# Performance work log

Hardware: AMD Instinct MI355X
Metric: run time of the kernel (lower is better)

Reference implementation:

```python
import jax, jax.numpy as jnp
import numpy as np

HEADS = 12
EPS = 1e-5

def setup_inputs() -> dict:
    key = jax.random.key(0)
    ks = jax.random.split(key, 24)
    B, T, H = 128, 128, 768
    RIN, RH, NT = 512, 512, 10
    s = 0.02
    inp = {
        'slot_vector': jax.random.normal(ks[0], (B, H), jnp.float32),
        'utt_vectors': jax.random.normal(ks[1], (B, T, H), jnp.float32),
        'Wq': jax.random.normal(ks[2], (H, H), jnp.float32) * s,
        'bq': jnp.zeros((H,), jnp.float32),
        'Wk': jax.random.normal(ks[3], (H, H), jnp.float32) * s,
        'bk': jnp.zeros((H,), jnp.float32),
        'Wv': jax.random.normal(ks[4], (H, H), jnp.float32) * s,
        'bv': jnp.zeros((H,), jnp.float32),
        'Wo': jax.random.normal(ks[5], (H, H), jnp.float32) * s,
        'bo': jnp.zeros((H,), jnp.float32),
        'W_in': jax.random.normal(ks[6], (RIN, 2 * H), jnp.float32) * s,
        'b_in': jnp.zeros((RIN,), jnp.float32),
        'W_ih': jax.random.normal(ks[7], (4 * RH, RIN), jnp.float32) * s,
        'W_hh': jax.random.normal(ks[8], (4 * RH, RH), jnp.float32) * s,
        'b_ih': jnp.zeros((4 * RH,), jnp.float32),
        'b_hh': jnp.zeros((4 * RH,), jnp.float32),
        'W_tag': jax.random.normal(ks[9], (NT, RH), jnp.float32) * s,
        'b_tag': jnp.zeros((NT,), jnp.float32),
        'ln_g': jnp.ones((NT,), jnp.float32),
        'ln_b': jnp.zeros((NT,), jnp.float32),
    }
    return inp

def _forward(slot_vector, utt_vectors, Wq, bq, Wk, bk, Wv, bv, Wo, bo,
             W_in, b_in, W_ih, W_hh, b_ih, b_hh, W_tag, b_tag, ln_g, ln_b):
    B, T, H = utt_vectors.shape
    dk = H // HEADS
    # Multi-head attention: Q is slot vector (seq len 1), K/V are utt encodings
    q = (slot_vector @ Wq.T + bq).reshape(B, 1, HEADS, dk).transpose(0, 2, 1, 3)  # [B,h,1,dk]
    k = (utt_vectors @ Wk.T + bk).reshape(B, T, HEADS, dk).transpose(0, 2, 1, 3)  # [B,h,T,dk]
    v = (utt_vectors @ Wv.T + bv).reshape(B, T, HEADS, dk).transpose(0, 2, 1, 3)
    scores = jnp.einsum('bhqd,bhkd->bhqk', q, k) / jnp.sqrt(jnp.float32(dk))
    attn = jax.nn.softmax(scores, axis=-1)
    X = jnp.einsum('bhqk,bhkd->bhqd', attn, v).transpose(0, 2, 1, 3).reshape(B, H)
    X = X @ Wo.T + bo  # [B, H] context vector, fixed across timesteps
    RH = W_hh.shape[1]
    h0 = jnp.zeros((B, RH), jnp.float32)
    c0 = jnp.zeros((B, RH), jnp.float32)

    def step(carry, x_t):
        h, c = carry
        lstm_in = jax.nn.sigmoid(jnp.concatenate([x_t, X], axis=1) @ W_in.T + b_in)
        gates = lstm_in @ W_ih.T + b_ih + h @ W_hh.T + b_hh  # [B, 4*RH]
        i_g, f_g, g_g, o_g = jnp.split(gates, 4, axis=1)  # torch gate order i,f,g,o
        c = jax.nn.sigmoid(f_g) * c + jax.nn.sigmoid(i_g) * jnp.tanh(g_g)
        h = jax.nn.sigmoid(o_g) * jnp.tanh(c)
        y = h @ W_tag.T + b_tag  # [B, NT]
        mu = jnp.mean(y, axis=-1, keepdims=True)
        var = jnp.mean((y - mu) ** 2, axis=-1, keepdims=True)
        y = (y - mu) / jnp.sqrt(var + EPS) * ln_g + ln_b
        return (h, c), y

    xs = utt_vectors.transpose(1, 0, 2)  # [T, B, H]
    _, ys = jax.lax.scan(step, (h0, c0), xs)  # ys: [T, B, NT]
    return ys.transpose(1, 2, 0)  # [B, NT, T]

def reference(slot_vector, utt_vectors, Wq, bq, Wk, bk, Wv, bv, Wo, bo,
              W_in, b_in, W_ih, W_hh, b_ih, b_hh, W_tag, b_tag, ln_g, ln_b):
    return _forward(slot_vector, utt_vectors, Wq, bq, Wk, bk, Wv, bv, Wo, bo,
                    W_in, b_in, W_ih, W_hh, b_ih, b_hh, W_tag, b_tag, ln_g, ln_b)
```

## Files before the change

kernel.cpp:

```cpp
#include <hip/hip_runtime.h>
#include <hip/hip_bf16.h>
#include <math.h>

#define Bc 128
#define Tc 128
#define Hc 768
#define NHEAD 12
#define DKc 64
#define RHc 512
#define G4c 2048
#define NTc 10
#define LNEPS 1e-5f
#define NSLC 16

typedef short bf16x8 __attribute__((ext_vector_type(8)));
typedef float f32x4 __attribute__((ext_vector_type(4)));

__device__ __forceinline__ float sigmoidf_(float x) { return 1.0f / (1.0f + expf(-x)); }

__device__ __forceinline__ ushort f2bf(float f) {
  union { float f; uint u; } c; c.f = f;
  uint r = (c.u + 0x7FFFu + ((c.u >> 16) & 1u)) >> 16;
  return (ushort)r;
}
__device__ __forceinline__ float bf2f(ushort u) {
  union { uint u; float f; } c; c.u = ((uint)u) << 16;
  return c.f;
}
__device__ __forceinline__ uint pack2(float a, float b) {
  return (uint)f2bf(a) | ((uint)f2bf(b) << 16);
}

__global__ void bias_sum_k(const float* __restrict__ a, const float* __restrict__ b,
                           float* __restrict__ o) {
  int i = blockIdx.x * blockDim.x + threadIdx.x;
  if (i < G4c) o[i] = a[i] + b[i];
}

__global__ void cvt4_k(const float* __restrict__ x, ushort* __restrict__ y, int n4) {
  int i = blockIdx.x * 256 + threadIdx.x;
  if (i < n4) {
    float4 v = ((const float4*)x)[i];
    ushort4 o; o.x = f2bf(v.x); o.y = f2bf(v.y); o.z = f2bf(v.z); o.w = f2bf(v.w);
    ((ushort4*)y)[i] = o;
  }
}

__global__ __launch_bounds__(256) void cvt_whh_frag_k(
    const float* __restrict__ Whh, ushort* __restrict__ out)
{
  const int idx = blockIdx.x * 256 + threadIdx.x;
  const int lane = idx & 63;
  const int kf = (idx >> 6) & 15;
  const int sw = idx >> 10;
  const int m = lane & 15;
  const int u = (sw >> 3) * 32 + (sw & 7) * 4 + (m >> 2);
  const int gate = m & 3;
  const int k0 = kf * 32 + (lane >> 4) * 8;
  const float* src = Whh + ((size_t)(gate * RHc + u)) * RHc + k0;
  ushort4 o0, o1;
  o0.x = f2bf(src[0]); o0.y = f2bf(src[1]); o0.z = f2bf(src[2]); o0.w = f2bf(src[3]);
  o1.x = f2bf(src[4]); o1.y = f2bf(src[5]); o1.z = f2bf(src[6]); o1.w = f2bf(src[7]);
  ushort* dst = out + (size_t)idx * 8;
  *(ushort4*)dst = o0;
  *(ushort4*)(dst + 4) = o1;
}

__global__ __launch_bounds__(256) void bgemm_bt(
    const void* __restrict__ Aptr, const ushort* __restrict__ Wb,
    const float* __restrict__ bias, void* __restrict__ Cptr,
    int M, int N, int K, int amode, int outMode,
    const float* __restrict__ utt, const float* __restrict__ xo, int trow0)
{
  __shared__ ushort As[128 * 40];
  __shared__ ushort Ws[128 * 40];
  const int tid = threadIdx.x;
  const int lane = tid & 63, wid = tid >> 6;
  const int wm = wid >> 1, wn = wid & 1;
  const int row0 = blockIdx.y * 128, col0 = blockIdx.x * 128;

  f32x4 acc[4][4];
#pragma unroll
  for (int i = 0; i < 4; ++i)
#pragma unroll
    for (int j = 0; j < 4; ++j) {
      f32x4 z = {0.f, 0.f, 0.f, 0.f};
      acc[i][j] = z;
    }

  const int r = tid >> 1, kq = (tid & 1) * 16;

  for (int kb = 0; kb < K; kb += 32) {
    const int k = kb + kq;
    if (amode == 2) {
      const ushort* ap = (const ushort*)Aptr + (size_t)(row0 + r) * K + k;
      *(uint4*)&As[r * 40 + kq] = *(const uint4*)ap;
      *(uint4*)&As[r * 40 + kq + 8] = *(const uint4*)(ap + 8);
    } else {
      const float* ap;
      if (amode == 0) {
        ap = (const float*)Aptr + (size_t)(row0 + r) * K + k;
      } else {
        const int b = r;
        const int t = trow0 + blockIdx.y;
        ap = (k < Hc) ? utt + ((size_t)b * Tc + t) * Hc + k
                      : xo + (size_t)b * Hc + (k - Hc);
      }
      const float4 f0 = *(const float4*)ap;
      const float4 f1 = *(const float4*)(ap + 4);
      const float4 f2 = *(const float4*)(ap + 8);
      const float4 f3 = *(const float4*)(ap + 12);
      uint4 u0, u1;
      u0.x = pack2(f0.x, f0.y); u0.y = pack2(f0.z, f0.w);
      u0.z = pack2(f1.x, f1.y); u0.w = pack2(f1.z, f1.w);
      u1.x = pack2(f2.x, f2.y); u1.y = pack2(f2.z, f2.w);
      u1.z = pack2(f3.x, f3.y); u1.w = pack2(f3.z, f3.w);
      *(uint4*)&As[r * 40 + kq] = u0;
      *(uint4*)&As[r * 40 + kq + 8] = u1;
    }
    {
      const ushort* wp = Wb + (size_t)(col0 + r) * K + k;
      *(uint4*)&Ws[r * 40 + kq] = *(const uint4*)wp;
      *(uint4*)&Ws[r * 40 + kq + 8] = *(const uint4*)(wp + 8);
    }
    __syncthreads();
    const int koff = (lane >> 4) * 8;
    const int ar = wm * 64 + (lane & 15);
    const int wr = wn * 64 + (lane & 15);
    bf16x8 af[4], wf[4];
#pragma unroll
    for (int i = 0; i < 4; ++i) af[i] = *(const bf16x8*)&As[(ar + i * 16) * 40 + koff];
#pragma unroll
    for (int i = 0; i < 4; ++i) wf[i] = *(const bf16x8*)&Ws[(wr + i * 16) * 40 + koff];
#pragma unroll
    for (int fm = 0; fm < 4; ++fm)
#pragma unroll
      for (int fn = 0; fn < 4; ++fn)
        acc[fm][fn] = __builtin_amdgcn_mfma_f32_16x16x32_bf16(af[fm], wf[fn], acc[fm][fn], 0, 0, 0);
    __syncthreads();
  }

#pragma unroll
  for (int fm = 0; fm < 4; ++fm) {
    const int m0 = row0 + wm * 64 + fm * 16 + ((lane >> 4) * 4);
#pragma unroll
    for (int fn = 0; fn < 4; ++fn) {
      const int n = col0 + wn * 64 + fn * 16 + (lane & 15);
      const float bb = bias[n];
#pragma unroll
      for (int q = 0; q < 4; ++q) {
        const float v = acc[fm][fn][q] + bb;
        if (outMode == 1)
          ((ushort*)Cptr)[(size_t)(m0 + q) * N + n] = f2bf(sigmoidf_(v));
        else
          ((float*)Cptr)[(size_t)(m0 + q) * N + n] = v;
      }
    }
  }
}

__global__ __launch_bounds__(256) void fold_qp_k(
    const float* __restrict__ slot, const float* __restrict__ Wq,
    const float* __restrict__ bq, const float* __restrict__ Wk,
    const float* __restrict__ bk, ushort* __restrict__ Pb, float* __restrict__ cqB)
{
  __shared__ float ss[Hc];
  __shared__ float qp[4][DKc];
  __shared__ float qs[DKc];
  const int bx = blockIdx.x;
  const int b = bx / NHEAD, h = bx % NHEAD;
  const int tid = threadIdx.x;
  for (int i = tid; i < Hc; i += 256) ss[i] = slot[(size_t)b * Hc + i];
  __syncthreads();
  {
    const int d = tid & 63, qt = tid >> 6;
    const float* wr = Wq + (size_t)(h * DKc + d) * Hc + qt * 192;
    const float* sb = ss + qt * 192;
    float a = 0.f;
    for (int e = 0; e < 192; e += 4) {
      const float4 wv = *(const float4*)(wr + e);
      a += wv.x * sb[e] + wv.y * sb[e + 1] + wv.z * sb[e + 2] + wv.w * sb[e + 3];
    }
    qp[qt][d] = a;
  }
  __syncthreads();
  if (tid < DKc)
    qs[tid] = qp[0][tid] + qp[1][tid] + qp[2][tid] + qp[3][tid] + bq[h * DKc + tid];
  __syncthreads();
  if (tid < DKc) {
    float pv = qs[tid] * bk[h * DKc + tid];
#pragma unroll
    for (int off = 32; off; off >>= 1) pv += __shfl_xor(pv, off);
    if (tid == 0) cqB[b * NHEAD + h] = pv;
  }
  for (int j = tid; j < Hc; j += 256) {
    float a = 0.f;
#pragma unroll 8
    for (int d = 0; d < DKc; ++d)
      a = fmaf(qs[d], Wk[(size_t)(h * DKc + d) * Hc + j], a);
    Pb[((size_t)b * NHEAD + h) * Hc + j] = f2bf(a);
  }
}

__global__ __launch_bounds__(256) void attn_scores2_k(
    const ushort* __restrict__ Pb, const float* __restrict__ cqB,
    const float* __restrict__ utt, float* __restrict__ Att)
{
  __shared__ float Phs[NHEAD][Hc];
  __shared__ float sc[NHEAD][Tc];
  const int b = blockIdx.x;
  const int tid = threadIdx.x;
  for (int i = tid; i < NHEAD * Hc; i += 256)
    ((float*)Phs)[i] = bf2f(Pb[(size_t)b * NHEAD * Hc + i]);
  __syncthreads();
  const int t = tid & 127, hh = tid >> 7;
  const int h0 = hh * 6;
  float a6[6];
#pragma unroll
  for (int i = 0; i < 6; ++i) a6[i] = 0.f;
  const float* xr = utt + ((size_t)b * Tc + t) * Hc;
  for (int j = 0; j < Hc; j += 4) {
    const float4 xv = *(const float4*)(xr + j);
#pragma unroll
    for (int i = 0; i < 6; ++i) {
      a6[i] = fmaf(xv.x, Phs[h0 + i][j], a6[i]);
      a6[i] = fmaf(xv.y, Phs[h0 + i][j + 1], a6[i]);
      a6[i] = fmaf(xv.z, Phs[h0 + i][j + 2], a6[i]);
      a6[i] = fmaf(xv.w, Phs[h0 + i][j + 3], a6[i]);
    }
  }
#pragma unroll
  for (int i = 0; i < 6; ++i)
    sc[h0 + i][t] = (a6[i] + cqB[b * NHEAD + h0 + i]) * 0.125f;
  __syncthreads();
  const int w = tid >> 6, lane = tid & 63;
#pragma unroll
  for (int i = 0; i < 3; ++i) {
    const int h = w * 3 + i;
    const float s0 = sc[h][lane], s1 = sc[h][lane + 64];
    float m = fmaxf(s0, s1);
#pragma unroll
    for (int off = 32; off; off >>= 1) m = fmaxf(m, __shfl_xor(m, off));
    const float e0 = expf(s0 - m), e1 = expf(s1 - m);
    float s = e0 + e1;
#pragma unroll
    for (int off = 32; off; off >>= 1) s += __shfl_xor(s, off);
    const float inv = 1.f / s;
    Att[((size_t)b * NHEAD + h) * Tc + lane] = e0 * inv;
    Att[((size_t)b * NHEAD + h) * Tc + lane + 64] = e1 * inv;
  }
}

__global__ __launch_bounds__(256) void attn_uxc_k(
    const float* __restrict__ Att, const float* __restrict__ utt,
    const float* __restrict__ Wv, const float* __restrict__ bv,
    float* __restrict__ Xc)
{
  __shared__ float As[NHEAD][Tc];
  __shared__ float Us[NHEAD * Hc];
  const int b = blockIdx.x;
  const int tid = threadIdx.x;
  for (int i = tid; i < NHEAD * Tc; i += 256)
    ((float*)As)[i] = Att[(size_t)b * NHEAD * Tc + i];
  __syncthreads();
  float acc[NHEAD][3];
#pragma unroll
  for (int h = 0; h < NHEAD; ++h)
#pragma unroll
    for (int q = 0; q < 3; ++q) acc[h][q] = 0.f;
  for (int t = 0; t < Tc; ++t) {
    const float* xr = utt + ((size_t)b * Tc + t) * Hc;
    const float x0 = xr[tid], x1 = xr[tid + 256], x2 = xr[tid + 512];
#pragma unroll
    for (int h = 0; h < NHEAD; ++h) {
      const float a = As[h][t];
      acc[h][0] = fmaf(a, x0, acc[h][0]);
      acc[h][1] = fmaf(a, x1, acc[h][1]);
      acc[h][2] = fmaf(a, x2, acc[h][2]);
    }
  }
#pragma unroll
  for (int h = 0; h < NHEAD; ++h)
#pragma unroll
    for (int q = 0; q < 3; ++q)
      Us[h * Hc + tid + q * 256] = acc[h][q];
  __syncthreads();
#pragma unroll
  for (int rr = 0; rr < 3; ++rr) {
    const int hd = tid + rr * 256;
    const int h = hd >> 6;
    const float* wr = Wv + (size_t)hd * Hc;
    const float* ub = Us + h * Hc;
    float a = 0.f;
    for (int j = 0; j < Hc; j += 4) {
      const float4 w4 = *(const float4*)(wr + j);
      a += w4.x * ub[j] + w4.y * ub[j + 1] + w4.z * ub[j + 2] + w4.w * ub[j + 3];
    }
    Xc[(size_t)b * Hc + hd] = a + bv[hd];
  }
}

__device__ __forceinline__ void group_barrier(unsigned* line) {
  __syncthreads();
  if (threadIdx.x == 0) {
    __builtin_amdgcn_fence(__ATOMIC_RELEASE, "agent");
    unsigned g = __hip_atomic_load(line + 1, __ATOMIC_RELAXED, __HIP_MEMORY_SCOPE_AGENT);
    unsigned a = __hip_atomic_fetch_add(line, 1u, __ATOMIC_ACQ_REL, __HIP_MEMORY_SCOPE_AGENT);
    if (a == NSLC - 1) {
      __hip_atomic_store(line, 0u, __ATOMIC_RELAXED, __HIP_MEMORY_SCOPE_AGENT);
      __hip_atomic_store(line + 1, g + 1u, __ATOMIC_RELEASE, __HIP_MEMORY_SCOPE_AGENT);
    } else {
      while (__hip_atomic_load(line + 1, __ATOMIC_RELAXED, __HIP_MEMORY_SCOPE_AGENT) == g)
        __builtin_amdgcn_s_sleep(1);
      __builtin_amdgcn_fence(__ATOMIC_ACQUIRE, "agent");
    }
  }
  __syncthreads();
}

__global__ __launch_bounds__(512, 1) void lstm_mfma_k(
    const ushort* __restrict__ WhhF, const float* __restrict__ GXc,
    ushort* __restrict__ hbuf, float* __restrict__ Hch,
    float* __restrict__ Cb, int t0, int nsteps, unsigned* __restrict__ bars)
{
  __shared__ ushort hs[16 * 520];
  const int blk = blockIdx.x;
  const int gid = blk >> 4, sid = blk & 15;
  const int tid = threadIdx.x;
  const int w = tid >> 6, lane = tid & 63;
  const int bl = lane & 15, uq = lane >> 4;
  const int uglob = sid * 32 + w * 4 + uq;
  const int bglob = gid * 16 + bl;
  unsigned* line = bars + gid * 32;

  bf16x8 afr[16];
  {
    const ushort* base = WhhF + ((size_t)((sid * 8 + w) * 16) * 64 + lane) * 8;
#pragma unroll
    for (int kf = 0; kf < 16; ++kf)
      afr[kf] = *(const bf16x8*)(base + (size_t)kf * 64 * 8);
  }

  float creg = (t0 > 0) ? Cb[(size_t)bglob * RHc + uglob] : 0.f;
  ushort* hbg = hbuf + (size_t)gid * (2 * 16 * RHc);

  for (int s = 0; s < nsteps; ++s) {
    const int t = t0 + s;
    const float* gx = GXc + ((size_t)s * Bc + bglob) * G4c + uglob;
    const float g0 = gx[0], g1 = gx[512], g2 = gx[1024], g3 = gx[1536];
    f32x4 acc = {0.f, 0.f, 0.f, 0.f};
    if (t > 0) {
      {
        const int b = tid >> 5, u0 = (tid & 31) * 16;
        const ushort* src = hbg + (size_t)((t & 1) ^ 1) * (16 * RHc) + b * RHc + u0;
        uint4 v0 = *(const uint4*)src;
        uint4 v1 = *(const uint4*)(src + 8);
        *(uint4*)&hs[b * 520 + u0] = v0;
        *(uint4*)&hs[b * 520 + u0 + 8] = v1;
      }
      __syncthreads();
#pragma unroll
      for (int kf = 0; kf < 16; ++kf) {
        const bf16x8 bf = *(const bf16x8*)&hs[bl * 520 + kf * 32 + uq * 8];
        acc = __builtin_amdgcn_mfma_f32_16x16x32_bf16(afr[kf], bf, acc, 0, 0, 0);
      }
    }
    const float gi = g0 + acc[0];
    const float gf = g1 + acc[1];
    const float gg = g2 + acc[2];
    const float go = g3 + acc[3];
    const float iv = sigmoidf_(gi);
    const float fv = sigmoidf_(gf);
    const float gv = tanhf(gg);
    const float ov = sigmoidf_(go);
    creg = fmaf(fv, creg, iv * gv);
    const float hval = ov * tanhf(creg);
    hbg[(size_t)(t & 1) * (16 * RHc) + bl * RHc + uglob] = f2bf(hval);
    Hch[((size_t)s * Bc + bglob) * RHc + uglob] = hval;
    if (s != nsteps - 1) group_barrier(line);
  }
  Cb[(size_t)bglob * RHc + uglob] = creg;
}

__global__ __launch_bounds__(256) void tag_ln_k(
    const float* __restrict__ Hch, const float* __restrict__ Wtag,
    const float* __restrict__ btag, const float* __restrict__ lng,
    const float* __restrict__ lnb, float* __restrict__ out, int t0)
{
  const int wid = (blockIdx.x * blockDim.x + threadIdx.x) >> 6;
  const int lane = threadIdx.x & 63;
  const int tl = wid >> 7, b = wid & 127;
  const int t = t0 + tl;
  const float* hp = Hch + ((size_t)tl * Bc + b) * RHc;
  float y[NTc];
#pragma unroll
  for (int j = 0; j < NTc; ++j) y[j] = 0.f;
  for (int k = lane; k < RHc; k += 64) {
    const float hv = hp[k];
#pragma unroll
    for (int j = 0; j < NTc; ++j)
      y[j] = fmaf(hv, Wtag[(size_t)j * RHc + k], y[j]);
  }
#pragma unroll
  for (int off = 32; off > 0; off >>= 1)
#pragma unroll
    for (int j = 0; j < NTc; ++j)
      y[j] += __shfl_xor(y[j], off);
  float mu = 0.f;
#pragma unroll
  for (int j = 0; j < NTc; ++j) { y[j] += btag[j]; mu += y[j]; }
  mu *= (1.0f / NTc);
  float var = 0.f;
#pragma unroll
  for (int j = 0; j < NTc; ++j) { const float d = y[j] - mu; var = fmaf(d, d, var); }
  var *= (1.0f / NTc);
  const float inv = rsqrtf(var + LNEPS);
  if (lane < NTc) {
    out[(size_t)b * NTc * Tc + (size_t)lane * Tc + t] =
        (y[lane] - mu) * inv * lng[lane] + lnb[lane];
  }
}

extern "C" void kernel_launch(void* const* d_in, const int* in_sizes, int n_in,
                              void* d_out, int out_size, void* d_ws, size_t ws_size,
                              hipStream_t stream)
{
  const float* slot = (const float*)d_in[0];
  const float* utt  = (const float*)d_in[1];
  const float* Wq = (const float*)d_in[2];   const float* bq = (const float*)d_in[3];
  const float* Wk = (const float*)d_in[4];   const float* bk = (const float*)d_in[5];
  const float* Wv = (const float*)d_in[6];   const float* bv = (const float*)d_in[7];
  const float* Wo = (const float*)d_in[8];   const float* bo = (const float*)d_in[9];
  const float* W_in = (const float*)d_in[10]; const float* b_in = (const float*)d_in[11];
  const float* W_ih = (const float*)d_in[12]; const float* W_hh = (const float*)d_in[13];
  const float* b_ih = (const float*)d_in[14]; const float* b_hh = (const float*)d_in[15];
  const float* W_tag = (const float*)d_in[16]; const float* b_tag = (const float*)d_in[17];
  const float* ln_g = (const float*)d_in[18]; const float* ln_b = (const float*)d_in[19];
  float* out = (float*)d_out;
  float* ws = (float*)d_ws;

  int CHT = 16;
  while (CHT > 2 && 4ull * (2265088ull + 360448ull * (unsigned)CHT) > ws_size)
    CHT >>= 1;
  const int NCH = Tc / CHT;

  float* Xc    = ws;
  float* Xo    = Xc + 98304;
  float* bsum  = Xo + 98304;
  float* Cb    = bsum + 2048;
  float* Att   = Cb + 65536;
  ushort* hbuf = (ushort*)(Att + 196608);
  ushort* WinB = (ushort*)(ws + 526336);
  ushort* WihB = (ushort*)(ws + 919552);
  ushort* WoB  = (ushort*)(ws + 1443840);
  ushort* WhhF = (ushort*)(ws + 1738752);
  float* cqB   = ws + 2263040;
  unsigned* bars = (unsigned*)(ws + 2264576);
  ushort* LINc = (ushort*)(ws + 2265088);
  float* GXc   = ws + 2265088 + (size_t)32768 * CHT;
  float* Hch   = GXc + (size_t)262144 * CHT;
  ushort* Pb   = (ushort*)(ws + 2265088);

  (void)hipMemsetAsync(bars, 0, 2048, stream);

  hipLaunchKernelGGL(cvt4_k, dim3(768), dim3(256), 0, stream, W_in, WinB, 196608);
  hipLaunchKernelGGL(cvt4_k, dim3(1024), dim3(256), 0, stream, W_ih, WihB, 262144);
  hipLaunchKernelGGL(cvt4_k, dim3(576), dim3(256), 0, stream, Wo, WoB, 147456);
  hipLaunchKernelGGL(cvt_whh_frag_k, dim3(512), dim3(256), 0, stream, W_hh, WhhF);
  hipLaunchKernelGGL(bias_sum_k, dim3(8), dim3(256), 0, stream, b_ih, b_hh, bsum);

  hipLaunchKernelGGL(fold_qp_k, dim3(Bc * NHEAD), dim3(256), 0, stream,
                     slot, Wq, bq, Wk, bk, Pb, cqB);
  hipLaunchKernelGGL(attn_scores2_k, dim3(Bc), dim3(256), 0, stream, Pb, cqB, utt, Att);
  hipLaunchKernelGGL(attn_uxc_k, dim3(Bc), dim3(256), 0, stream, Att, utt, Wv, bv, Xc);
  hipLaunchKernelGGL(bgemm_bt, dim3(6, 1), dim3(256), 0, stream,
                     (const void*)Xc, WoB, bo, (void*)Xo, 128, 768, 768, 0, 0,
                     (const float*)nullptr, (const float*)nullptr, 0);

  for (int tc = 0; tc < NCH; ++tc) {
    hipLaunchKernelGGL(bgemm_bt, dim3(4, CHT), dim3(256), 0, stream,
                       (const void*)nullptr, WinB, b_in, (void*)LINc,
                       CHT * Bc, 512, 1536, 1, 1, utt, Xo, tc * CHT);
    hipLaunchKernelGGL(bgemm_bt, dim3(16, CHT), dim3(256), 0, stream,
                       (const void*)LINc, WihB, bsum, (void*)GXc,
                       CHT * Bc, 2048, 512, 2, 0,
                       (const float*)nullptr, (const float*)nullptr, 0);
    hipLaunchKernelGGL(lstm_mfma_k, dim3(128), dim3(512), 0, stream,
                       WhhF, GXc, hbuf, Hch, Cb, tc * CHT, CHT, bars);
    hipLaunchKernelGGL(tag_ln_k, dim3(CHT * 32), dim3(256), 0, stream,
                       Hch, W_tag, b_tag, ln_g, ln_b, out, tc * CHT);
  }
}
```

Measured before the change: 2.384 ms.

## Interleave LSTM gate columns, read h from global directly, prefetch gate inputs

Permutes the W_ih rows and the summed bias so the four gate preactivations for each hidden unit sit next to each other. The recurrent kernel can then load them as one float4 and prefetch the next step's values before the group barrier. The LDS staging of h and its __syncthreads are dropped, so the MFMA B operands are read straight from global/L2, and the block-to-group mapping is interleaved. sigmoid switches to the fast __expf, which adds a small accuracy risk, and uncached global reads of h may cost more latency than the LDS path did.

Measured after the change: 2.344 ms. Within noise of the previous version (-1.6%).

```diff
diff --git a/kernel.cpp b/kernel.cpp
--- a/kernel.cpp
+++ b/kernel.cpp
@@ -16,7 +16,7 @@
 typedef short bf16x8 __attribute__((ext_vector_type(8)));
 typedef float f32x4 __attribute__((ext_vector_type(4)));
 
-__device__ __forceinline__ float sigmoidf_(float x) { return 1.0f / (1.0f + expf(-x)); }
+__device__ __forceinline__ float sigmoidf_(float x) { return 1.0f / (1.0f + __expf(-x)); }
 
 __device__ __forceinline__ ushort f2bf(float f) {
   union { float f; uint u; } c; c.f = f;
@@ -31,10 +31,13 @@
   return (uint)f2bf(a) | ((uint)f2bf(b) << 16);
 }
 
-__global__ void bias_sum_k(const float* __restrict__ a, const float* __restrict__ b,
-                           float* __restrict__ o) {
+__global__ void bias_sum_perm_k(const float* __restrict__ a, const float* __restrict__ b,
+                                float* __restrict__ o) {
   int i = blockIdx.x * blockDim.x + threadIdx.x;
-  if (i < G4c) o[i] = a[i] + b[i];
+  if (i < G4c) {
+    const int g = i >> 9, u = i & 511;
+    o[u * 4 + g] = a[i] + b[i];
+  }
 }
 
 __global__ void cvt4_k(const float* __restrict__ x, ushort* __restrict__ y, int n4) {
@@ -44,6 +47,16 @@
     ushort4 o; o.x = f2bf(v.x); o.y = f2bf(v.y); o.z = f2bf(v.z); o.w = f2bf(v.w);
     ((ushort4*)y)[i] = o;
   }
+}
+
+__global__ __launch_bounds__(256) void cvt_wih_perm_k(
+    const float* __restrict__ W, ushort* __restrict__ out)
+{
+  const int rp = blockIdx.x;
+  const int u = rp >> 2, g = rp & 3;
+  const float* src = W + (size_t)(g * 512 + u) * 512;
+  ushort* dst = out + (size_t)rp * 512;
+  for (int k = threadIdx.x; k < 512; k += 256) dst[k] = f2bf(src[k]);
 }
 
 __global__ __launch_bounds__(256) void cvt_whh_frag_k(
@@ -323,9 +336,8 @@
     ushort* __restrict__ hbuf, float* __restrict__ Hch,
     float* __restrict__ Cb, int t0, int nsteps, unsigned* __restrict__ bars)
 {
-  __shared__ ushort hs[16 * 520];
   const int blk = blockIdx.x;
-  const int gid = blk >> 4, sid = blk & 15;
+  const int gid = blk & 7, sid = blk >> 3;
   const int tid = threadIdx.x;
   const int w = tid >> 6, lane = tid & 63;
   const int bl = lane & 15, uq = lane >> 4;
@@ -344,40 +356,35 @@
   float creg = (t0 > 0) ? Cb[(size_t)bglob * RHc + uglob] : 0.f;
   ushort* hbg = hbuf + (size_t)gid * (2 * 16 * RHc);
 
+  float4 gx4 = *(const float4*)(GXc + ((size_t)0 * Bc + bglob) * G4c + uglob * 4);
+
   for (int s = 0; s < nsteps; ++s) {
     const int t = t0 + s;
-    const float* gx = GXc + ((size_t)s * Bc + bglob) * G4c + uglob;
-    const float g0 = gx[0], g1 = gx[512], g2 = gx[1024], g3 = gx[1536];
     f32x4 acc = {0.f, 0.f, 0.f, 0.f};
     if (t > 0) {
-      {
-        const int b = tid >> 5, u0 = (tid & 31) * 16;
-        const ushort* src = hbg + (size_t)((t & 1) ^ 1) * (16 * RHc) + b * RHc + u0;
-        uint4 v0 = *(const uint4*)src;
-        uint4 v1 = *(const uint4*)(src + 8);
-        *(uint4*)&hs[b * 520 + u0] = v0;
-        *(uint4*)&hs[b * 520 + u0 + 8] = v1;
-      }
-      __syncthreads();
+      const ushort* hsrc = hbg + (size_t)((t & 1) ^ 1) * (16 * RHc) + (size_t)bl * RHc + uq * 8;
 #pragma unroll
       for (int kf = 0; kf < 16; ++kf) {
-        const bf16x8 bf = *(const bf16x8*)&hs[bl * 520 + kf * 32 + uq * 8];
+        const bf16x8 bf = *(const bf16x8*)(hsrc + kf * 32);
         acc = __builtin_amdgcn_mfma_f32_16x16x32_bf16(afr[kf], bf, acc, 0, 0, 0);
       }
     }
-    const float gi = g0 + acc[0];
-    const float gf = g1 + acc[1];
-    const float gg = g2 + acc[2];
-    const float go = g3 + acc[3];
+    const float gi = gx4.x + acc[0];
+    const float gf = gx4.y + acc[1];
+    const float gg = gx4.z + acc[2];
+    const float go = gx4.w + acc[3];
     const float iv = sigmoidf_(gi);
     const float fv = sigmoidf_(gf);
     const float gv = tanhf(gg);
     const float ov = sigmoidf_(go);
     creg = fmaf(fv, creg, iv * gv);
     const float hval = ov * tanhf(creg);
-    hbg[(size_t)(t & 1) * (16 * RHc) + bl * RHc + uglob] = f2bf(hval);
+    hbg[(size_t)(t & 1) * (16 * RHc) + (size_t)bl * RHc + uglob] = f2bf(hval);
     Hch[((size_t)s * Bc + bglob) * RHc + uglob] = hval;
-    if (s != nsteps - 1) group_barrier(line);
+    if (s != nsteps - 1) {
+      gx4 = *(const float4*)(GXc + ((size_t)(s + 1) * Bc + bglob) * G4c + uglob * 4);
+      group_barrier(line);
+    }
   }
   Cb[(size_t)bglob * RHc + uglob] = creg;
 }
@@ -464,10 +471,10 @@
   (void)hipMemsetAsync(bars, 0, 2048, stream);
 
   hipLaunchKernelGGL(cvt4_k, dim3(768), dim3(256), 0, stream, W_in, WinB, 196608);
-  hipLaunchKernelGGL(cvt4_k, dim3(1024), dim3(256), 0, stream, W_ih, WihB, 262144);
+  hipLaunchKernelGGL(cvt_wih_perm_k, dim3(2048), dim3(256), 0, stream, W_ih, WihB);
   hipLaunchKernelGGL(cvt4_k, dim3(576), dim3(256), 0, stream, Wo, WoB, 147456);
   hipLaunchKernelGGL(cvt_whh_frag_k, dim3(512), dim3(256), 0, stream, W_hh, WhhF);
-  hipLaunchKernelGGL(bias_sum_k, dim3(8), dim3(256), 0, stream, b_ih, b_hh, bsum);
+  hipLaunchKernelGGL(bias_sum_perm_k, dim3(8), dim3(256), 0, stream, b_ih, b_hh, bsum);
 
   hipLaunchKernelGGL(fold_qp_k, dim3(Bc * NHEAD), dim3(256), 0, stream,
                      slot, Wq, bq, Wk, bk, Pb, cqB);
```
